# Performance work log

Hardware: AMD Instinct MI355X
Metric: run time of the kernel (lower is better)

## Reference

```python
import jax, jax.numpy as jnp
import numpy as np

EPS = 0.01  # smoothing constant from the original module


def setup_inputs() -> dict:
    key = jax.random.key(0)
    k1, k2, k3, k4 = jax.random.split(key, 4)
    N, C, H, W = 8, 16, 512, 512
    pred = jax.random.uniform(k1, (N, C, H, W), dtype=jnp.float32)
    label = jax.random.randint(k2, (N, C, H, W), 0, 2, dtype=jnp.int32)
    Wl = jax.random.uniform(k3, (C,), dtype=jnp.float32)
    label_sum = jnp.ones((C,), dtype=jnp.float32)
    existmap = jax.random.uniform(k4, (N, C, H, W), dtype=jnp.float32)
    return {"pred": pred, "label": label, "Wl": Wl,
            "label_sum": label_sum, "existmap": existmap}


def reference(pred, label, Wl, label_sum, existmap):
    # Original loops over classes i, gathers pred[:, i] where label[:, i] == 1,
    # accumulates Wl[i] * sum(-log(p + 0.01) * existmap). Classes with an empty
    # mask contribute 0, so the vectorized masked form is exactly equivalent
    # (weight_exist=True path).
    mask = (label == 1).astype(pred.dtype)               # [N,C,H,W]
    per_elem = -jnp.log(pred + EPS) * existmap * mask    # fused elementwise
    loss = jnp.einsum('nchw,c->', per_elem, Wl) / jnp.sum(label_sum)
    return loss
```

## Files before the change

### kernel.cpp

```cpp
#include <hip/hip_runtime.h>


constexpr int BLOCK = 256;
constexpr int NBLK  = 2048;

__global__ __launch_bounds__(BLOCK) void lc_partial(
    const float4* __restrict__ pred,
    const int4*   __restrict__ label,
    const float*  __restrict__ Wl,
    const float4* __restrict__ exist,
    float* __restrict__ partials,
    int nvec)
{
    int tid    = blockIdx.x * BLOCK + threadIdx.x;
    int stride = gridDim.x * BLOCK;

    float acc = 0.f;
    for (int i = tid; i < nvec; i += stride) {
        float4 p = pred[i];
        int4   l = label[i];
        float4 e = exist[i];
        float w = Wl[(i >> 16) & 15];
        float s = 0.f;
        s += (l.x == 1) ? __logf(p.x + 0.01f) * e.x : 0.f;
        s += (l.y == 1) ? __logf(p.y + 0.01f) * e.y : 0.f;
        s += (l.z == 1) ? __logf(p.z + 0.01f) * e.z : 0.f;
        s += (l.w == 1) ? __logf(p.w + 0.01f) * e.w : 0.f;
        acc -= w * s;
    }

    #pragma unroll
    for (int off = 32; off > 0; off >>= 1)
        acc += __shfl_down(acc, off, 64);

    __shared__ float red[BLOCK / 64];
    int lane = threadIdx.x & 63;
    int wid  = threadIdx.x >> 6;
    if (lane == 0) red[wid] = acc;
    __syncthreads();
    if (threadIdx.x == 0) {
        float s = 0.f;
        #pragma unroll
        for (int i = 0; i < BLOCK / 64; ++i) s += red[i];
        partials[blockIdx.x] = s;
    }
}

__global__ __launch_bounds__(BLOCK) void lc_final(
    const float* __restrict__ partials,
    const float* __restrict__ label_sum,
    float* __restrict__ out,
    int nblk, int nls)
{
    float acc = 0.f;
    for (int i = threadIdx.x; i < nblk; i += BLOCK) acc += partials[i];

    #pragma unroll
    for (int off = 32; off > 0; off >>= 1)
        acc += __shfl_down(acc, off, 64);

    __shared__ float red[BLOCK / 64];
    int lane = threadIdx.x & 63;
    int wid  = threadIdx.x >> 6;
    if (lane == 0) red[wid] = acc;
    __syncthreads();
    if (threadIdx.x == 0) {
        float s = 0.f;
        #pragma unroll
        for (int i = 0; i < BLOCK / 64; ++i) s += red[i];
        float ls = 0.f;
        for (int i = 0; i < nls; ++i) ls += label_sum[i];
        out[0] = s / ls;
    }
}

extern "C" void kernel_launch(void* const* d_in, const int* in_sizes, int n_in,
                              void* d_out, int out_size, void* d_ws, size_t ws_size,
                              hipStream_t stream) {
    const float4* pred      = (const float4*)d_in[0];
    const int4*   label     = (const int4*)d_in[1];
    const float*  Wl        = (const float*)d_in[2];
    const float*  label_sum = (const float*)d_in[3];
    const float4* exist     = (const float4*)d_in[4];
    float* out = (float*)d_out;

    int nvec = in_sizes[0] / 4;
    int nls  = in_sizes[3];

    float* partials = (float*)d_ws;

    int grid = (nvec + BLOCK - 1) / BLOCK;
    if (grid > NBLK) grid = NBLK;

    lc_partial<<<grid, BLOCK, 0, stream>>>(pred, label, Wl, exist, partials, nvec);
    lc_final<<<1, BLOCK, 0, stream>>>(partials, label_sum, out, grid, nls);
}
```

Baseline: 354.6 us.

## Give each block a contiguous class-aligned chunk and hoist class weight

Swaps the grid-stride loop for fixed contiguous chunks of 2048 vectors per block, so each block covers a single class. The class weight is then loaded once per block and applied to the block partial instead of on every element. The loop is unrolled by two with separate accumulators to keep more loads in flight. This raises the grid from 2048 to 4096 blocks, and the per-block weight is only correct if chunks never cross a class boundary, which holds because 65536 is a multiple of 2048.

```diff
diff --git a/kernel.cpp b/kernel.cpp
--- a/kernel.cpp
+++ b/kernel.cpp
@@ -2,7 +2,7 @@
 
 
 constexpr int BLOCK = 256;
-constexpr int NBLK  = 2048;
+constexpr int WVEC  = 2048;
 
 __global__ __launch_bounds__(BLOCK) void lc_partial(
     const float4* __restrict__ pred,
@@ -12,22 +12,47 @@
     float* __restrict__ partials,
     int nvec)
 {
-    int tid    = blockIdx.x * BLOCK + threadIdx.x;
-    int stride = gridDim.x * BLOCK;
+    const int base = blockIdx.x * WVEC;
+    const int end  = min(base + WVEC, nvec);
 
-    float acc = 0.f;
-    for (int i = tid; i < nvec; i += stride) {
+    const float w = Wl[(base >> 16) & 15];
+
+    float acc0 = 0.f, acc1 = 0.f;
+
+    int i = base + threadIdx.x;
+    for (; i + BLOCK < end; i += 2 * BLOCK) {
+        float4 p0 = pred[i];
+        float4 p1 = pred[i + BLOCK];
+        int4   l0 = label[i];
+        int4   l1 = label[i + BLOCK];
+        float4 e0 = exist[i];
+        float4 e1 = exist[i + BLOCK];
+
+        float s0 = 0.f, s1 = 0.f;
+        s0 += (l0.x == 1) ? __logf(p0.x + 0.01f) * e0.x : 0.f;
+        s0 += (l0.y == 1) ? __logf(p0.y + 0.01f) * e0.y : 0.f;
+        s0 += (l0.z == 1) ? __logf(p0.z + 0.01f) * e0.z : 0.f;
+        s0 += (l0.w == 1) ? __logf(p0.w + 0.01f) * e0.w : 0.f;
+        s1 += (l1.x == 1) ? __logf(p1.x + 0.01f) * e1.x : 0.f;
+        s1 += (l1.y == 1) ? __logf(p1.y + 0.01f) * e1.y : 0.f;
+        s1 += (l1.z == 1) ? __logf(p1.z + 0.01f) * e1.z : 0.f;
+        s1 += (l1.w == 1) ? __logf(p1.w + 0.01f) * e1.w : 0.f;
+        acc0 += s0;
+        acc1 += s1;
+    }
+    if (i < end) {
         float4 p = pred[i];
         int4   l = label[i];
         float4 e = exist[i];
-        float w = Wl[(i >> 16) & 15];
-        float s = 0.f;
+        float  s = 0.f;
         s += (l.x == 1) ? __logf(p.x + 0.01f) * e.x : 0.f;
         s += (l.y == 1) ? __logf(p.y + 0.01f) * e.y : 0.f;
         s += (l.z == 1) ? __logf(p.z + 0.01f) * e.z : 0.f;
         s += (l.w == 1) ? __logf(p.w + 0.01f) * e.w : 0.f;
-        acc -= w * s;
+        acc0 += s;
     }
+
+    float acc = acc0 + acc1;
 
     #pragma unroll
     for (int off = 32; off > 0; off >>= 1)
@@ -41,8 +66,8 @@
     if (threadIdx.x == 0) {
         float s = 0.f;
         #pragma unroll
-        for (int i = 0; i < BLOCK / 64; ++i) s += red[i];
-        partials[blockIdx.x] = s;
+        for (int k = 0; k < BLOCK / 64; ++k) s += red[k];
+        partials[blockIdx.x] = -w * s;
     }
 }
 
@@ -67,7 +92,7 @@
     if (threadIdx.x == 0) {
         float s = 0.f;
         #pragma unroll
-        for (int i = 0; i < BLOCK / 64; ++i) s += red[i];
+        for (int k = 0; k < BLOCK / 64; ++k) s += red[k];
         float ls = 0.f;
         for (int i = 0; i < nls; ++i) ls += label_sum[i];
         out[0] = s / ls;
@@ -89,8 +114,7 @@
 
     float* partials = (float*)d_ws;
 
-    int grid = (nvec + BLOCK - 1) / BLOCK;
-    if (grid > NBLK) grid = NBLK;
+    int grid = (nvec + WVEC - 1) / WVEC;
 
     lc_partial<<<grid, BLOCK, 0, stream>>>(pred, label, Wl, exist, partials, nvec);
     lc_final<<<1, BLOCK, 0, stream>>>(partials, label_sum, out, grid, nls);
```

Result: no change. 354.0 us (-0.2%).
